# Optimization experiments

Hardware: AMD Instinct MI355X
Metric: run time of the kernel (lower is better)

## Reference

```python
import jax, jax.numpy as jnp
import numpy as np

D_MODEL = 32
D_STATE = 16
D_CONV = 4
D_INNER = 64  # expand * d_model
DT_RANK = 2   # ceil(d_model / 16)


def silu(x):
    return x * jax.nn.sigmoid(x)


def _mamba_params(key, scale=0.05):
    ks = jax.random.split(key, 7)
    p = {}
    p['in_w'] = jax.random.normal(ks[0], (2 * D_INNER, D_MODEL), jnp.float32) * scale
    p['conv_w'] = jax.random.normal(ks[1], (D_INNER, 1, D_CONV), jnp.float32) * scale
    p['conv_b'] = jax.random.normal(ks[2], (D_INNER,), jnp.float32) * scale
    p['xproj_w'] = jax.random.normal(ks[3], (DT_RANK + 2 * D_STATE, D_INNER), jnp.float32) * scale
    p['dt_w'] = jax.random.normal(ks[4], (D_INNER, DT_RANK), jnp.float32) * scale
    p['dt_b'] = jax.random.normal(ks[5], (D_INNER,), jnp.float32) * scale
    # S4D-real init: A = [1..d_state] broadcast over d_inner
    p['A_log'] = jnp.log(jnp.broadcast_to(jnp.arange(1, D_STATE + 1, dtype=jnp.float32), (D_INNER, D_STATE)))
    p['D'] = jnp.ones((D_INNER,), jnp.float32)
    p['out_w'] = jax.random.normal(ks[6], (D_MODEL, D_INNER), jnp.float32) * scale
    return p


def mamba(x, in_w, conv_w, conv_b, xproj_w, dt_w, dt_b, A_log, Dp, out_w):
    # x: (B, L, d_model)
    Bsz, L, _ = x.shape
    xz = x @ in_w.T                                   # (B, L, 2*d_inner)
    xi, z = jnp.split(xz, 2, axis=-1)
    # causal depthwise conv over L
    xc = jnp.pad(xi.transpose(0, 2, 1), ((0, 0), (0, 0), (D_CONV - 1, 0)))  # (B, d_inner, L+3)
    xc = jax.lax.conv_general_dilated(xc, conv_w, (1,), 'VALID',
                                      dimension_numbers=('NCH', 'OIH', 'NCH'),
                                      feature_group_count=D_INNER)
    xi = silu(xc.transpose(0, 2, 1) + conv_b)          # (B, L, d_inner)
    dbc = xi @ xproj_w.T                               # (B, L, dt_rank + 2*d_state)
    dt = dbc[..., :DT_RANK]
    Bm = dbc[..., DT_RANK:DT_RANK + D_STATE]           # (B, L, d_state)
    Cm = dbc[..., DT_RANK + D_STATE:]                  # (B, L, d_state)
    delta = jax.nn.softplus(dt @ dt_w.T + dt_b)        # (B, L, d_inner)
    A = -jnp.exp(A_log)                                # (d_inner, d_state)
    deltaA = jnp.exp(delta[..., None] * A)             # (B, L, d_inner, d_state)
    deltaBx = delta[..., None] * Bm[:, :, None, :] * xi[..., None]

    def step(h, t):
        dA, dBx = t
        h = dA * h + dBx
        return h, h

    h0 = jnp.zeros((Bsz, D_INNER, D_STATE), x.dtype)
    _, hs = jax.lax.scan(step, h0, (deltaA.transpose(1, 0, 2, 3), deltaBx.transpose(1, 0, 2, 3)))
    hs = hs.transpose(1, 0, 2, 3)                      # (B, L, d_inner, d_state)
    y = jnp.einsum('blds,bls->bld', hs, Cm) + Dp * xi
    y = y * silu(z)
    return y @ out_w.T                                 # (B, L, d_model)


def setup_inputs() -> dict:
    key = jax.random.key(0)
    ks = jax.random.split(key, 12)
    s = 0.05
    inp = {'inputs': jax.random.normal(ks[0], (32, 512, 64, 64), jnp.float32)}
    inp['proj_avg_w'] = jax.random.normal(ks[1], (D_MODEL, 1), jnp.float32) * s
    inp['proj_avg_b'] = jax.random.normal(ks[2], (D_MODEL,), jnp.float32) * s
    inp['proj_max_w'] = jax.random.normal(ks[3], (D_MODEL, 1), jnp.float32) * s
    inp['proj_max_b'] = jax.random.normal(ks[4], (D_MODEL,), jnp.float32) * s
    inp['gate_w'] = jax.random.normal(ks[5], (1, 2), jnp.float32) * s
    inp['gate_b'] = jax.random.normal(ks[6], (1,), jnp.float32) * s
    inp['out_w'] = jax.random.normal(ks[7], (1, D_MODEL), jnp.float32) * s
    inp['out_b'] = jax.random.normal(ks[8], (1,), jnp.float32) * s
    pf = _mamba_params(ks[9])
    pb = _mamba_params(ks[10])
    for k, v in pf.items():
        inp['f_' + k] = v
    for k, v in pb.items():
        inp['b_' + k] = v
    return inp


def reference(inputs, proj_avg_w, proj_avg_b, proj_max_w, proj_max_b, gate_w, gate_b,
              out_w, out_b,
              f_in_w, f_conv_w, f_conv_b, f_xproj_w, f_dt_w, f_dt_b, f_A_log, f_D, f_out_w,
              b_in_w, b_conv_w, b_conv_b, b_xproj_w, b_dt_w, b_dt_b, b_A_log, b_D, b_out_w):
    # global avg / max pool -> (B, C, 1)
    x_avg = jnp.mean(inputs, axis=(2, 3))[..., None]
    x_max = jnp.max(inputs, axis=(2, 3))[..., None]
    gate_in = jnp.concatenate([x_avg, x_max], axis=-1)            # (B, C, 2)
    alpha = jax.nn.sigmoid(gate_in @ gate_w.T + gate_b)           # (B, C, 1)
    xa = x_avg @ proj_avg_w.T + proj_avg_b                        # (B, C, d_model)
    xm = x_max @ proj_max_w.T + proj_max_b
    fwd = (f_in_w, f_conv_w, f_conv_b, f_xproj_w, f_dt_w, f_dt_b, f_A_log, f_D, f_out_w)
    bwd = (b_in_w, b_conv_w, b_conv_b, b_xproj_w, b_dt_w, b_dt_b, b_A_log, b_D, b_out_w)
    y_avg = mamba(xa, *fwd) + jnp.flip(mamba(jnp.flip(xa, 1), *bwd), 1)
    y_max = mamba(xm, *fwd) + jnp.flip(mamba(jnp.flip(xm, 1), *bwd), 1)
    y = alpha * y_avg + (1.0 - alpha) * y_max
    att = jax.nn.sigmoid(y @ out_w.T + out_b)                     # (B, C, 1)
    return att[..., None]                                         # (B, C, 1, 1)
```

## Files before the change

kernel.cpp:

```cpp
#include <hip/hip_runtime.h>
#include <math.h>

#define OFF_YPART 32768
#define OFF_PD    294912
#define OFF_PX    (OFF_PD + 4194304)
#define OFF_PG    (OFF_PX + 4194304)
#define OFF_BCB   (OFF_PG + 4194304)
#define OFF_BCC   (OFF_BCB + 524288)
#define OFF_YB    (OFF_BCC + 524288)

__global__ __launch_bounds__(256) void kreduce(const float* __restrict__ in,
                                               float* __restrict__ xavg,
                                               float* __restrict__ xmax) {
    const int bl = blockIdx.x;
    const float* p = in + (size_t)bl * 4096;
    const int t = threadIdx.x;
    float s = 0.f, m = -INFINITY;
#pragma unroll
    for (int it = 0; it < 4; ++it) {
        float4 v = *reinterpret_cast<const float4*>(p + (size_t)(it * 256 + t) * 4);
        s += v.x + v.y + v.z + v.w;
        m = fmaxf(m, fmaxf(fmaxf(v.x, v.y), fmaxf(v.z, v.w)));
    }
#pragma unroll
    for (int o = 1; o < 64; o <<= 1) {
        s += __shfl_xor(s, o);
        m = fmaxf(m, __shfl_xor(m, o));
    }
    __shared__ float ls[4], lm[4];
    const int w = t >> 6;
    if ((t & 63) == 0) { ls[w] = s; lm[w] = m; }
    __syncthreads();
    if (t == 0) {
        s = ls[0] + ls[1] + ls[2] + ls[3];
        m = fmaxf(fmaxf(lm[0], lm[1]), fmaxf(lm[2], lm[3]));
        xavg[bl] = s * (1.f / 4096.f);
        xmax[bl] = m;
    }
}

__device__ __forceinline__ int dbc_slot(int j) {
    return j < 2 ? j : (j < 18 ? 2 * j - 2 : 2 * j - 33);
}

__global__ __launch_bounds__(512) void kprep(
    const float* __restrict__ xavg, const float* __restrict__ xmax,
    float* __restrict__ ws,
    const float* __restrict__ paw, const float* __restrict__ pab,
    const float* __restrict__ pmw, const float* __restrict__ pmb,
    const float* __restrict__ outw_outer,
    const float* __restrict__ f_in_w, const float* __restrict__ f_conv_w,
    const float* __restrict__ f_conv_b, const float* __restrict__ f_xproj_w,
    const float* __restrict__ f_dt_w, const float* __restrict__ f_dt_b,
    const float* __restrict__ f_D, const float* __restrict__ f_out_w,
    const float* __restrict__ b_in_w, const float* __restrict__ b_conv_w,
    const float* __restrict__ b_conv_b, const float* __restrict__ b_xproj_w,
    const float* __restrict__ b_dt_w, const float* __restrict__ b_dt_b,
    const float* __restrict__ b_D, const float* __restrict__ b_out_w)
{
    const int tid = threadIdx.x;
    const int c  = blockIdx.x >> 8;
    const int b  = (blockIdx.x >> 3) & 31;
    const int cq = blockIdx.x & 7;
    const int strm = c >> 1, dir = c & 1;

    const float* in_w = dir ? b_in_w   : f_in_w;
    const float* cwp  = dir ? b_conv_w : f_conv_w;
    const float* cbp  = dir ? b_conv_b : f_conv_b;
    const float* xpw  = dir ? b_xproj_w: f_xproj_w;
    const float* dtwp = dir ? b_dt_w   : f_dt_w;
    const float* dtbp = dir ? b_dt_b   : f_dt_b;
    const float* Dpar = dir ? b_D      : f_D;
    const float* owp  = dir ? b_out_w  : f_out_w;
    const float* projw = strm ? pmw : paw;
    const float* projb = strm ? pmb : pab;
    const float* xin   = strm ? xmax : xavg;

    __shared__ float sseq4[68];
    __shared__ float su[128], sv[128];
    __shared__ float scw[64][4], scb[64], sdtw[64][2], sdtb[64], sD[64], swf[64];
    __shared__ float sxp[34][68];
    __shared__ float sxi[64][68];
    __shared__ float sdbc[64][37];

    if (tid < 67) {
        int g = cq * 64 - 3 + tid;
        float val = 0.f;
        if (g >= 0) val = xin[b * 512 + (dir ? (511 - g) : g)];
        sseq4[tid] = val;
    }
    if (tid < 128) {
        float u = 0.f, v = 0.f;
        const float* row = in_w + tid * 32;
#pragma unroll
        for (int m = 0; m < 32; ++m) {
            u = fmaf(row[m], projw[m], u);
            v = fmaf(row[m], projb[m], v);
        }
        su[tid] = u; sv[tid] = v;
    }
    if (tid < 64) {
#pragma unroll
        for (int k = 0; k < 4; ++k) scw[tid][k] = cwp[tid * 4 + k];
        scb[tid] = cbp[tid];
        sdtw[tid][0] = dtwp[tid * 2];
        sdtw[tid][1] = dtwp[tid * 2 + 1];
        sdtb[tid] = dtbp[tid];
        sD[tid] = Dpar[tid];
        float wf = 0.f;
#pragma unroll
        for (int m = 0; m < 32; ++m) wf = fmaf(outw_outer[m], owp[m * 64 + tid], wf);
        swf[tid] = wf;
    }
    for (int i = tid; i < 34 * 64; i += 512) sxp[i >> 6][i & 63] = xpw[i];
    __syncthreads();

    const int ll8 = tid >> 3;
    const int j8  = tid & 7;
    const int gi  = cq * 64 + ll8;

    {
        float t0 = sseq4[ll8], t1 = sseq4[ll8 + 1], t2 = sseq4[ll8 + 2], t3 = sseq4[ll8 + 3];
        float vv0 = (gi >= 3) ? 1.f : 0.f;
        float vv1 = (gi >= 2) ? 1.f : 0.f;
        float vv2 = (gi >= 1) ? 1.f : 0.f;
#pragma unroll
        for (int k = 0; k < 8; ++k) {
            int di = j8 * 8 + k;
            float u = su[di], v = sv[di];
            float xc = scw[di][0] * fmaf(t0, u, vv0 * v)
                     + scw[di][1] * fmaf(t1, u, vv1 * v)
                     + scw[di][2] * fmaf(t2, u, vv2 * v)
                     + scw[di][3] * fmaf(t3, u, v);
            xc += scb[di];
            float sig = 1.f / (1.f + __expf(-xc));
            sxi[ll8][di] = xc * sig;
        }
    }
    __syncthreads();

    {
        float a0 = 0.f, a1 = 0.f, a2 = 0.f, a3 = 0.f, a4 = 0.f;
        const float4* xr4 = reinterpret_cast<const float4*>(&sxi[ll8][0]);
        const float4* r0 = reinterpret_cast<const float4*>(&sxp[j8 + 0][0]);
        const float4* r1 = reinterpret_cast<const float4*>(&sxp[j8 + 8][0]);
        const float4* r2 = reinterpret_cast<const float4*>(&sxp[j8 + 16][0]);
        const float4* r3 = reinterpret_cast<const float4*>(&sxp[j8 + 24][0]);
        const float4* r4 = (j8 < 2) ? reinterpret_cast<const float4*>(&sxp[j8 + 32][0]) : r0;
        bool extra = (j8 < 2);
#pragma unroll 2
        for (int q = 0; q < 16; ++q) {
            float4 x = xr4[q];
            float4 w;
            w = r0[q]; a0 = fmaf(x.x,w.x,fmaf(x.y,w.y,fmaf(x.z,w.z,fmaf(x.w,w.w,a0))));
            w = r1[q]; a1 = fmaf(x.x,w.x,fmaf(x.y,w.y,fmaf(x.z,w.z,fmaf(x.w,w.w,a1))));
            w = r2[q]; a2 = fmaf(x.x,w.x,fmaf(x.y,w.y,fmaf(x.z,w.z,fmaf(x.w,w.w,a2))));
            w = r3[q]; a3 = fmaf(x.x,w.x,fmaf(x.y,w.y,fmaf(x.z,w.z,fmaf(x.w,w.w,a3))));
            if (extra) { w = r4[q]; a4 = fmaf(x.x,w.x,fmaf(x.y,w.y,fmaf(x.z,w.z,fmaf(x.w,w.w,a4)))); }
        }
        sdbc[ll8][dbc_slot(j8)]      = a0;
        sdbc[ll8][dbc_slot(j8 + 8)]  = a1;
        sdbc[ll8][dbc_slot(j8 + 16)] = a2;
        sdbc[ll8][dbc_slot(j8 + 24)] = a3;
        if (extra) sdbc[ll8][dbc_slot(j8 + 32)] = a4;
    }
    __syncthreads();

    {
        const size_t tile = ((size_t)(c * 32 + b) * 8 + cq) * 4096;
        float dt0 = sdbc[ll8][0], dt1 = sdbc[ll8][1];
        float x3 = sseq4[ll8 + 3];
        float ybp = 0.f;
#pragma unroll 2
        for (int k = 0; k < 8; ++k) {
            int di = j8 * 8 + k;
            float xi = sxi[ll8][di];
            float pre = fmaf(dt0, sdtw[di][0], fmaf(dt1, sdtw[di][1], sdtb[di]));
            float sp = (pre > 20.f) ? pre : __logf(1.f + __expf(pre));
            float zv = fmaf(x3, su[64 + di], sv[64 + di]);
            float g = (zv / (1.f + __expf(-zv))) * swf[di];
            ws[OFF_PD + tile + di * 64 + ll8] = sp;
            ws[OFF_PX + tile + di * 64 + ll8] = sp * xi;
            ws[OFF_PG + tile + di * 64 + ll8] = g;
            ybp = fmaf(g * sD[di], xi, ybp);
        }
        ybp += __shfl_xor(ybp, 1);
        ybp += __shfl_xor(ybp, 2);
        ybp += __shfl_xor(ybp, 4);
        if (j8 == 0) ws[OFF_YB + (size_t)(c * 32 + b) * 512 + gi] = ybp;
    }

    {
        const size_t bb = ((size_t)(c * 32 + b) * 8 + cq) * 1024;
        for (int i = tid; i < 1024; i += 512) {
            int s = i >> 6, t = i & 63;
            ws[OFF_BCB + bb + i] = sdbc[t][2 + 2 * s];
            ws[OFF_BCC + bb + i] = sdbc[t][3 + 2 * s];
        }
    }
}

#define DPP_ADD(v, ctrl) ((v) + __int_as_float(__builtin_amdgcn_update_dpp(0, __float_as_int(v), (ctrl), 0xF, 0xF, true)))

__global__ __launch_bounds__(256) void kscan(
    float* __restrict__ ws,
    const float* __restrict__ f_A_log, const float* __restrict__ b_A_log)
{
    const int tid = threadIdx.x;
    const int c  = blockIdx.x >> 7;
    const int dq = (blockIdx.x >> 5) & 3;
    const int b  = blockIdx.x & 31;
    const int dir = c & 1;
    const float* alog = dir ? b_A_log : f_A_log;

    const int dd = tid >> 4;
    const int s  = tid & 15;
    const int d  = dq * 16 + dd;
    const float cA = -expf(alog[d * 16 + s]) * 1.44269504088896340736f;
    float h = 0.f;

    __shared__ float sd[16][68], sx[16][68], sg[16][68];
    __shared__ float sB[16][68], sC[16][68];
    __shared__ float syT[16][68];
    __shared__ float syb[64];

    const int srow = tid >> 4;
    const int scol = (tid & 15) * 4;
    float* ypart = ws + OFF_YPART;

    for (int chunk = 0; chunk < 8; ++chunk) {
        const size_t tb = (size_t)(c * 32 + b) * 8 + chunk;
        const float* pd = ws + OFF_PD + tb * 4096 + dq * 1024;
        const float* px = ws + OFF_PX + tb * 4096 + dq * 1024;
        const float* pg = ws + OFF_PG + tb * 4096 + dq * 1024;
        const float* pB = ws + OFF_BCB + tb * 1024;
        const float* pC = ws + OFF_BCC + tb * 1024;

        *reinterpret_cast<float4*>(&sd[srow][scol]) =
            *reinterpret_cast<const float4*>(pd + srow * 64 + scol);
        *reinterpret_cast<float4*>(&sx[srow][scol]) =
            *reinterpret_cast<const float4*>(px + srow * 64 + scol);
        *reinterpret_cast<float4*>(&sg[srow][scol]) =
            *reinterpret_cast<const float4*>(pg + srow * 64 + scol);
        *reinterpret_cast<float4*>(&sB[srow][scol]) =
            *reinterpret_cast<const float4*>(pB + srow * 64 + scol);
        *reinterpret_cast<float4*>(&sC[srow][scol]) =
            *reinterpret_cast<const float4*>(pC + srow * 64 + scol);
        if (dq == 0 && tid < 64) syb[tid] = ws[OFF_YB + (size_t)(c * 32 + b) * 512 + chunk * 64 + tid];
        __syncthreads();

        {
#pragma unroll 2
            for (int m = 0; m < 16; ++m) {
                float4 de = *reinterpret_cast<const float4*>(&sd[dd][4 * m]);
                float4 dx = *reinterpret_cast<const float4*>(&sx[dd][4 * m]);
                float4 gq = *reinterpret_cast<const float4*>(&sg[dd][4 * m]);
                float4 Bq = *reinterpret_cast<const float4*>(&sB[s][4 * m]);
                float4 Cq = *reinterpret_cast<const float4*>(&sC[s][4 * m]);
                float4 val;
                float a, pc;
                a = exp2f(de.x * cA); h = fmaf(a, h, dx.x * Bq.x); pc = h * Cq.x;
                pc = DPP_ADD(pc, 0x101); pc = DPP_ADD(pc, 0x102);
                pc = DPP_ADD(pc, 0x104); pc = DPP_ADD(pc, 0x108);
                val.x = pc * gq.x;
                a = exp2f(de.y * cA); h = fmaf(a, h, dx.y * Bq.y); pc = h * Cq.y;
                pc = DPP_ADD(pc, 0x101); pc = DPP_ADD(pc, 0x102);
                pc = DPP_ADD(pc, 0x104); pc = DPP_ADD(pc, 0x108);
                val.y = pc * gq.y;
                a = exp2f(de.z * cA); h = fmaf(a, h, dx.z * Bq.z); pc = h * Cq.z;
                pc = DPP_ADD(pc, 0x101); pc = DPP_ADD(pc, 0x102);
                pc = DPP_ADD(pc, 0x104); pc = DPP_ADD(pc, 0x108);
                val.z = pc * gq.z;
                a = exp2f(de.w * cA); h = fmaf(a, h, dx.w * Bq.w); pc = h * Cq.w;
                pc = DPP_ADD(pc, 0x101); pc = DPP_ADD(pc, 0x102);
                pc = DPP_ADD(pc, 0x104); pc = DPP_ADD(pc, 0x108);
                val.w = pc * gq.w;
                if (s == 0) *reinterpret_cast<float4*>(&syT[dd][4 * m]) = val;
            }
        }
        __syncthreads();

        {
            const int tt4 = tid >> 2;
            const int j4  = tid & 3;
            float acc = syT[j4 * 4][tt4] + syT[j4 * 4 + 1][tt4]
                      + syT[j4 * 4 + 2][tt4] + syT[j4 * 4 + 3][tt4];
            acc += __shfl_xor(acc, 1);
            acc += __shfl_xor(acc, 2);
            if (j4 == 0) {
                int i = chunk * 64 + tt4;
                int l = dir ? (511 - i) : i;
                float res = acc + (dq == 0 ? syb[tt4] : 0.f);
                ypart[((c * 4 + dq) * 32 + b) * 512 + l] = res;
            }
        }
        __syncthreads();
    }
}

__global__ __launch_bounds__(256) void kfinal(const float* __restrict__ xavg,
                                              const float* __restrict__ xmax,
                                              const float* __restrict__ ypart,
                                              const float* __restrict__ gate_w,
                                              const float* __restrict__ gate_b,
                                              const float* __restrict__ out_b,
                                              float* __restrict__ out) {
    const int idx = blockIdx.x * 256 + threadIdx.x;
    float xa = xavg[idx], xm = xmax[idx];
    float alpha = 1.f / (1.f + __expf(-(fmaf(xa, gate_w[0], fmaf(xm, gate_w[1], gate_b[0])))));
    float sa = 0.f, sm = 0.f;
#pragma unroll
    for (int k = 0; k < 8; ++k)  sa += ypart[k * 16384 + idx];
#pragma unroll
    for (int k = 8; k < 16; ++k) sm += ypart[k * 16384 + idx];
    float y = alpha * sa + (1.f - alpha) * sm + out_b[0];
    out[idx] = 1.f / (1.f + __expf(-y));
}

extern "C" void kernel_launch(void* const* d_in, const int* in_sizes, int n_in,
                              void* d_out, int out_size, void* d_ws, size_t ws_size,
                              hipStream_t stream) {
    const float* inp = (const float*)d_in[0];
    const float* paw = (const float*)d_in[1];
    const float* pab = (const float*)d_in[2];
    const float* pmw = (const float*)d_in[3];
    const float* pmb = (const float*)d_in[4];
    const float* gw  = (const float*)d_in[5];
    const float* gb  = (const float*)d_in[6];
    const float* ow  = (const float*)d_in[7];
    const float* ob  = (const float*)d_in[8];

    float* ws = (float*)d_ws;
    float* xavg = ws;
    float* xmax = ws + 16384;
    float* ypart = ws + OFF_YPART;
    float* out = (float*)d_out;

    kreduce<<<16384, 256, 0, stream>>>(inp, xavg, xmax);
    kprep<<<1024, 512, 0, stream>>>(
        xavg, xmax, ws, paw, pab, pmw, pmb, ow,
        (const float*)d_in[9],  (const float*)d_in[10], (const float*)d_in[11], (const float*)d_in[12],
        (const float*)d_in[13], (const float*)d_in[14], (const float*)d_in[16], (const float*)d_in[17],
        (const float*)d_in[18], (const float*)d_in[19], (const float*)d_in[20], (const float*)d_in[21],
        (const float*)d_in[22], (const float*)d_in[23], (const float*)d_in[25], (const float*)d_in[26]);
    kscan<<<512, 256, 0, stream>>>(
        ws, (const float*)d_in[15], (const float*)d_in[24]);
    kfinal<<<64, 256, 0, stream>>>(xavg, xmax, ypart, gw, gb, ob, out);
}
```

Baseline: 126.0 us.

## Give each scan thread two state columns and halve the scan grid

The selective-scan kernel now assigns two of the sixteen state entries to each thread, so a block covers 32 inner channels instead of 16 and the grid drops from 512 to 256 blocks. This halves the cross-lane DPP reduction depth per step, removes duplicated B/C tile loads across blocks, and halves the partial-output buffers that the final kernel sums. In exchange, 256 blocks may underfill the device's compute units, and each thread carries a longer serial dependency chain.

New measurement: 133.3 us. +5.8%, slower.

```diff
diff --git a/kernel.cpp b/kernel.cpp
--- a/kernel.cpp
+++ b/kernel.cpp
@@ -207,46 +207,53 @@
     const float* __restrict__ f_A_log, const float* __restrict__ b_A_log)
 {
     const int tid = threadIdx.x;
-    const int c  = blockIdx.x >> 7;
-    const int dq = (blockIdx.x >> 5) & 3;
+    const int c  = blockIdx.x >> 6;
+    const int dh = (blockIdx.x >> 5) & 1;
     const int b  = blockIdx.x & 31;
     const int dir = c & 1;
     const float* alog = dir ? b_A_log : f_A_log;
 
-    const int dd = tid >> 4;
-    const int s  = tid & 15;
-    const int d  = dq * 16 + dd;
-    const float cA = -expf(alog[d * 16 + s]) * 1.44269504088896340736f;
-    float h = 0.f;
-
-    __shared__ float sd[16][68], sx[16][68], sg[16][68];
+    const int dd = tid >> 3;
+    const int s8 = tid & 7;
+    const int d  = dh * 32 + dd;
+    const float cA0 = -expf(alog[d * 16 + s8])     * 1.44269504088896340736f;
+    const float cA1 = -expf(alog[d * 16 + s8 + 8]) * 1.44269504088896340736f;
+    float h0 = 0.f, h1 = 0.f;
+
+    __shared__ float sd[32][68], sx[32][68], sg[32][68];
     __shared__ float sB[16][68], sC[16][68];
-    __shared__ float syT[16][68];
+    __shared__ float syT[32][68];
     __shared__ float syb[64];
 
-    const int srow = tid >> 4;
-    const int scol = (tid & 15) * 4;
+    const int row = tid >> 4;
+    const int col = (tid & 15) * 4;
     float* ypart = ws + OFF_YPART;
 
     for (int chunk = 0; chunk < 8; ++chunk) {
         const size_t tb = (size_t)(c * 32 + b) * 8 + chunk;
-        const float* pd = ws + OFF_PD + tb * 4096 + dq * 1024;
-        const float* px = ws + OFF_PX + tb * 4096 + dq * 1024;
-        const float* pg = ws + OFF_PG + tb * 4096 + dq * 1024;
+        const float* pd = ws + OFF_PD + tb * 4096 + dh * 2048;
+        const float* px = ws + OFF_PX + tb * 4096 + dh * 2048;
+        const float* pg = ws + OFF_PG + tb * 4096 + dh * 2048;
         const float* pB = ws + OFF_BCB + tb * 1024;
         const float* pC = ws + OFF_BCC + tb * 1024;
 
-        *reinterpret_cast<float4*>(&sd[srow][scol]) =
-            *reinterpret_cast<const float4*>(pd + srow * 64 + scol);
-        *reinterpret_cast<float4*>(&sx[srow][scol]) =
-            *reinterpret_cast<const float4*>(px + srow * 64 + scol);
-        *reinterpret_cast<float4*>(&sg[srow][scol]) =
-            *reinterpret_cast<const float4*>(pg + srow * 64 + scol);
-        *reinterpret_cast<float4*>(&sB[srow][scol]) =
-            *reinterpret_cast<const float4*>(pB + srow * 64 + scol);
-        *reinterpret_cast<float4*>(&sC[srow][scol]) =
-            *reinterpret_cast<const float4*>(pC + srow * 64 + scol);
-        if (dq == 0 && tid < 64) syb[tid] = ws[OFF_YB + (size_t)(c * 32 + b) * 512 + chunk * 64 + tid];
+        *reinterpret_cast<float4*>(&sd[row][col]) =
+            *reinterpret_cast<const float4*>(pd + row * 64 + col);
+        *reinterpret_cast<float4*>(&sd[row + 16][col]) =
+            *reinterpret_cast<const float4*>(pd + (row + 16) * 64 + col);
+        *reinterpret_cast<float4*>(&sx[row][col]) =
+            *reinterpret_cast<const float4*>(px + row * 64 + col);
+        *reinterpret_cast<float4*>(&sx[row + 16][col]) =
+            *reinterpret_cast<const float4*>(px + (row + 16) * 64 + col);
+        *reinterpret_cast<float4*>(&sg[row][col]) =
+            *reinterpret_cast<const float4*>(pg + row * 64 + col);
+        *reinterpret_cast<float4*>(&sg[row + 16][col]) =
+            *reinterpret_cast<const float4*>(pg + (row + 16) * 64 + col);
+        *reinterpret_cast<float4*>(&sB[row][col]) =
+            *reinterpret_cast<const float4*>(pB + row * 64 + col);
+        *reinterpret_cast<float4*>(&sC[row][col]) =
+            *reinterpret_cast<const float4*>(pC + row * 64 + col);
+        if (dh == 0 && tid < 64) syb[tid] = ws[OFF_YB + (size_t)(c * 32 + b) * 512 + chunk * 64 + tid];
         __syncthreads();
 
         {
@@ -255,27 +262,33 @@
                 float4 de = *reinterpret_cast<const float4*>(&sd[dd][4 * m]);
                 float4 dx = *reinterpret_cast<const float4*>(&sx[dd][4 * m]);
                 float4 gq = *reinterpret_cast<const float4*>(&sg[dd][4 * m]);
-                float4 Bq = *reinterpret_cast<const float4*>(&sB[s][4 * m]);
-                float4 Cq = *reinterpret_cast<const float4*>(&sC[s][4 * m]);
+                float4 B0 = *reinterpret_cast<const float4*>(&sB[s8][4 * m]);
+                float4 B1 = *reinterpret_cast<const float4*>(&sB[s8 + 8][4 * m]);
+                float4 C0 = *reinterpret_cast<const float4*>(&sC[s8][4 * m]);
+                float4 C1 = *reinterpret_cast<const float4*>(&sC[s8 + 8][4 * m]);
                 float4 val;
                 float a, pc;
-                a = exp2f(de.x * cA); h = fmaf(a, h, dx.x * Bq.x); pc = h * Cq.x;
-                pc = DPP_ADD(pc, 0x101); pc = DPP_ADD(pc, 0x102);
-                pc = DPP_ADD(pc, 0x104); pc = DPP_ADD(pc, 0x108);
+                a = exp2f(de.x * cA0); h0 = fmaf(a, h0, dx.x * B0.x);
+                a = exp2f(de.x * cA1); h1 = fmaf(a, h1, dx.x * B1.x);
+                pc = fmaf(h0, C0.x, h1 * C1.x);
+                pc = DPP_ADD(pc, 0x101); pc = DPP_ADD(pc, 0x102); pc = DPP_ADD(pc, 0x104);
                 val.x = pc * gq.x;
-                a = exp2f(de.y * cA); h = fmaf(a, h, dx.y * Bq.y); pc = h * Cq.y;
-                pc = DPP_ADD(pc, 0x101); pc = DPP_ADD(pc, 0x102);
-                pc = DPP_ADD(pc, 0x104); pc = DPP_ADD(pc, 0x108);
+                a = exp2f(de.y * cA0); h0 = fmaf(a, h0, dx.y * B0.y);
+                a = exp2f(de.y * cA1); h1 = fmaf(a, h1, dx.y * B1.y);
+                pc = fmaf(h0, C0.y, h1 * C1.y);
+                pc = DPP_ADD(pc, 0x101); pc = DPP_ADD(pc, 0x102); pc = DPP_ADD(pc, 0x104);
                 val.y = pc * gq.y;
-                a = exp2f(de.z * cA); h = fmaf(a, h, dx.z * Bq.z); pc = h * Cq.z;
-                pc = DPP_ADD(pc, 0x101); pc = DPP_ADD(pc, 0x102);
-                pc = DPP_ADD(pc, 0x104); pc = DPP_ADD(pc, 0x108);
+                a = exp2f(de.z * cA0); h0 = fmaf(a, h0, dx.z * B0.z);
+                a = exp2f(de.z * cA1); h1 = fmaf(a, h1, dx.z * B1.z);
+                pc = fmaf(h0, C0.z, h1 * C1.z);
+                pc = DPP_ADD(pc, 0x101); pc = DPP_ADD(pc, 0x102); pc = DPP_ADD(pc, 0x104);
                 val.z = pc * gq.z;
-                a = exp2f(de.w * cA); h = fmaf(a, h, dx.w * Bq.w); pc = h * Cq.w;
-                pc = DPP_ADD(pc, 0x101); pc = DPP_ADD(pc, 0x102);
-                pc = DPP_ADD(pc, 0x104); pc = DPP_ADD(pc, 0x108);
+                a = exp2f(de.w * cA0); h0 = fmaf(a, h0, dx.w * B0.w);
+                a = exp2f(de.w * cA1); h1 = fmaf(a, h1, dx.w * B1.w);
+                pc = fmaf(h0, C0.w, h1 * C1.w);
+                pc = DPP_ADD(pc, 0x101); pc = DPP_ADD(pc, 0x102); pc = DPP_ADD(pc, 0x104);
                 val.w = pc * gq.w;
-                if (s == 0) *reinterpret_cast<float4*>(&syT[dd][4 * m]) = val;
+                if (s8 == 0) *reinterpret_cast<float4*>(&syT[dd][4 * m]) = val;
             }
         }
         __syncthreads();
@@ -283,15 +296,16 @@
         {
             const int tt4 = tid >> 2;
             const int j4  = tid & 3;
-            float acc = syT[j4 * 4][tt4] + syT[j4 * 4 + 1][tt4]
-                      + syT[j4 * 4 + 2][tt4] + syT[j4 * 4 + 3][tt4];
+            float acc = 0.f;
+#pragma unroll
+            for (int k = 0; k < 8; ++k) acc += syT[j4 + 4 * k][tt4];
             acc += __shfl_xor(acc, 1);
             acc += __shfl_xor(acc, 2);
             if (j4 == 0) {
                 int i = chunk * 64 + tt4;
                 int l = dir ? (511 - i) : i;
-                float res = acc + (dq == 0 ? syb[tt4] : 0.f);
-                ypart[((c * 4 + dq) * 32 + b) * 512 + l] = res;
+                float res = acc + (dh == 0 ? syb[tt4] : 0.f);
+                ypart[((c * 2 + dh) * 32 + b) * 512 + l] = res;
             }
         }
         __syncthreads();
@@ -310,9 +324,9 @@
     float alpha = 1.f / (1.f + __expf(-(fmaf(xa, gate_w[0], fmaf(xm, gate_w[1], gate_b[0])))));
     float sa = 0.f, sm = 0.f;
 #pragma unroll
-    for (int k = 0; k < 8; ++k)  sa += ypart[k * 16384 + idx];
-#pragma unroll
-    for (int k = 8; k < 16; ++k) sm += ypart[k * 16384 + idx];
+    for (int k = 0; k < 4; ++k) sa += ypart[k * 16384 + idx];
+#pragma unroll
+    for (int k = 4; k < 8; ++k) sm += ypart[k * 16384 + idx];
     float y = alpha * sa + (1.f - alpha) * sm + out_b[0];
     out[idx] = 1.f / (1.f + __expf(-y));
 }
@@ -343,7 +357,7 @@
         (const float*)d_in[13], (const float*)d_in[14], (const float*)d_in[16], (const float*)d_in[17],
         (const float*)d_in[18], (const float*)d_in[19], (const float*)d_in[20], (const float*)d_in[21],
         (const float*)d_in[22], (const float*)d_in[23], (const float*)d_in[25], (const float*)d_in[26]);
-    kscan<<<512, 256, 0, stream>>>(
+    kscan<<<256, 256, 0, stream>>>(
         ws, (const float*)d_in[15], (const float*)d_in[24]);
     kfinal<<<64, 256, 0, stream>>>(xavg, xmax, ypart, gw, gb, ob, out);
 }
```
